# Optimization experiments

Measured on AMD Instinct MI355X. Metric: run time of the kernel, lower is better.

## Reference

```python
import jax, jax.numpy as jnp
import numpy as np

B, S, D, H = 2, 2048, 1024, 16
DK = D // H


def setup_inputs() -> dict:
    key = jax.random.key(0)
    ks = jax.random.split(key, 9)
    def xavier(k, shape):
        fan_in, fan_out = shape[1], shape[0]
        lim = jnp.sqrt(6.0 / (fan_in + fan_out))
        return jax.random.uniform(k, shape, jnp.float32, -lim, lim)
    x = jax.random.normal(ks[0], (B, S, D), jnp.float32)
    mask = jnp.ones((B, 1, S), jnp.int32)
    Wq = xavier(ks[1], (D, D)); bq = jnp.zeros((D,), jnp.float32)
    Wk = xavier(ks[2], (D, D)); bk = jnp.zeros((D,), jnp.float32)
    Wv = xavier(ks[3], (D, D)); bv = jnp.zeros((D,), jnp.float32)
    Wo = xavier(ks[4], (D, D)); bo = jnp.zeros((D,), jnp.float32)
    return {"x": x, "mask": mask, "Wq": Wq, "bq": bq, "Wk": Wk, "bk": bk,
            "Wv": Wv, "bv": bv, "Wo": Wo, "bo": bo}


def reference(x, mask, Wq, bq, Wk, bk, Wv, bv, Wo, bo):
    # Linear layers use torch convention y = x @ W.T + b
    q = (x @ Wq.T + bq).reshape(B, S, H, DK).transpose(0, 2, 1, 3)  # [B,H,S,DK]
    k = (x @ Wk.T + bk).reshape(B, S, H, DK).transpose(0, 2, 1, 3)
    v = (x @ Wv.T + bv).reshape(B, S, H, DK).transpose(0, 2, 1, 3)
    scores = jnp.einsum('bhqd,bhkd->bhqk', q, k) / jnp.sqrt(jnp.float32(DK))
    m = mask[:, None, :, :]  # unsqueeze(1): broadcast over heads -> [B,1,1,S]
    scores = jnp.where(m == 0, jnp.float32(-1e9), scores)
    p = jax.nn.softmax(scores, axis=-1)  # dropout p=0.0 -> identity
    ctx = jnp.einsum('bhqk,bhkd->bhqd', p, v)
    ctx = ctx.transpose(0, 2, 1, 3).reshape(B, S, D)
    return ctx @ Wo.T + bo
```

## Files before the change

### kernel.cpp

```cpp
#include <hip/hip_runtime.h>
#include <hip/hip_bf16.h>
#include <math.h>

#define Bn 2
#define Sn 2048
#define Dn 1024
#define Hn 16
#define DKn 64
#define BHS (Bn * Hn * Sn)

using fragb  = __attribute__((ext_vector_type(8))) short;
using frag16 = __attribute__((ext_vector_type(8))) _Float16;
using f4     = __attribute__((ext_vector_type(4))) float;

__device__ __forceinline__ short f2bf(float f) {
    union { float f; unsigned u; } v; v.f = f;
    unsigned r = v.u + 0x7FFF + ((v.u >> 16) & 1);
    return (short)(r >> 16);
}
__device__ __forceinline__ unsigned short f2h(float f) {
    _Float16 h = (_Float16)f;
    unsigned short s; __builtin_memcpy(&s, &h, 2); return s;
}

#define GLOAD(gptr, lptr)                                                     \
    __builtin_amdgcn_global_load_lds(                                         \
        (const __attribute__((address_space(1))) unsigned int*)(const void*)(gptr), \
        (__attribute__((address_space(3))) unsigned int*)(void*)(lptr), 16, 0, 0)

#define NX (Bn * Sn * Dn)
#define NW (Dn * Dn)
#define NF4 ((NX + 4 * NW) / 4)

__global__ __launch_bounds__(256) void prep(
    const float* __restrict__ x,  const float* __restrict__ Wq,
    const float* __restrict__ Wk, const float* __restrict__ Wv,
    const float* __restrict__ Wo, const int* __restrict__ mask,
    short* __restrict__ xh,
    short* __restrict__ Wqh, short* __restrict__ Wkh,
    short* __restrict__ Wvh, short* __restrict__ Woh,
    short* __restrict__ mfb)
{
    int i = blockIdx.x * 256 + threadIdx.x;
    if (i < NF4) {
        int e = i << 2;
        const float* src; short* dst; int j;
        if (e < NX)               { src = x;  dst = xh;  j = e; }
        else if (e < NX + NW)     { src = Wq; dst = Wqh; j = e - NX; }
        else if (e < NX + 2 * NW) { src = Wk; dst = Wkh; j = e - NX - NW; }
        else if (e < NX + 3 * NW) { src = Wv; dst = Wvh; j = e - NX - 2 * NW; }
        else                      { src = Wo; dst = Woh; j = e - NX - 3 * NW; }
        float4 v = *(const float4*)(src + j);
        ushort4 o;
        o.x = f2h(v.x); o.y = f2h(v.y); o.z = f2h(v.z); o.w = f2h(v.w);
        *(ushort4*)(dst + j) = o;
    } else {
        int j = (i - NF4) << 2;
        if (j < Bn * Sn) {
            int4 m = *(const int4*)(mask + j);
            ushort4 o;
            o.x = m.x ? 0x3F80 : 0; o.y = m.y ? 0x3F80 : 0;
            o.z = m.z ? 0x3F80 : 0; o.w = m.w ? 0x3F80 : 0;
            *(ushort4*)(mfb + j) = o;
        }
    }
}

__global__ __launch_bounds__(256) void gemm_qkv(
    const short* __restrict__ A,
    const short* __restrict__ W0, const float* __restrict__ b0,
    const short* __restrict__ W1, const float* __restrict__ b1,
    const short* __restrict__ W2, const float* __restrict__ b2,
    const int* __restrict__ mask,
    short* __restrict__ Qb, short* __restrict__ Kb, short* __restrict__ Vtb)
{
    __shared__ __align__(16) short As[128 * 32];
    __shared__ __align__(16) short Bs[128 * 32];

    const int tid  = threadIdx.x;
    const int wave = tid >> 6;
    const int lane = tid & 63;
    const int quad = lane >> 4;
    const int l16  = lane & 15;
    const int wm   = wave >> 1;
    const int wn   = wave & 1;

    const int m0   = blockIdx.y * 128;
    const int n0   = blockIdx.x * 128;
    const int widx = n0 >> 10;
    const int nl0  = n0 & 1023;

    const short* Wp   = widx == 0 ? W0 : (widx == 1 ? W1 : W2);
    const float* bias = widx == 0 ? b0 : (widx == 1 ? b1 : b2);

    f4 acc[4][4];
    #pragma unroll
    for (int i = 0; i < 4; i++)
        #pragma unroll
        for (int j = 0; j < 4; j++) {
            acc[i][j][0] = 0.f; acc[i][j][1] = 0.f;
            acc[i][j][2] = 0.f; acc[i][j][3] = 0.f;
        }

    const int K = Dn;
    const int r0  = tid >> 2,         kc0 = (tid & 3) * 8;
    const int r1  = (tid + 256) >> 2;
    const short* Ar0 = A  + (size_t)(m0 + r0) * K + kc0;
    const short* Ar1 = A  + (size_t)(m0 + r1) * K + kc0;
    const short* Br0 = Wp + (size_t)(nl0 + r0) * K + kc0;
    const short* Br1 = Wp + (size_t)(nl0 + r1) * K + kc0;

    for (int k0 = 0; k0 < K; k0 += 32) {
        __syncthreads();
        GLOAD(Ar0 + k0, &As[(wave * 64) * 8]);
        GLOAD(Ar1 + k0, &As[(256 + wave * 64) * 8]);
        GLOAD(Br0 + k0, &Bs[(wave * 64) * 8]);
        GLOAD(Br1 + k0, &Bs[(256 + wave * 64) * 8]);
        __syncthreads();

        frag16 a[4], b[4];
        #pragma unroll
        for (int mi = 0; mi < 4; mi++)
            a[mi] = *(const frag16*)&As[(wm * 64 + mi * 16 + l16) * 32 + quad * 8];
        #pragma unroll
        for (int ni = 0; ni < 4; ni++)
            b[ni] = *(const frag16*)&Bs[(wn * 64 + ni * 16 + l16) * 32 + quad * 8];
        #pragma unroll
        for (int mi = 0; mi < 4; mi++)
            #pragma unroll
            for (int ni = 0; ni < 4; ni++)
                acc[mi][ni] = __builtin_amdgcn_mfma_f32_16x16x32_f16(
                    a[mi], b[ni], acc[mi][ni], 0, 0, 0);
    }

    const float QSCALE = 0.125f * 1.44269504088896340736f;

    #pragma unroll
    for (int mi = 0; mi < 4; mi++) {
        #pragma unroll
        for (int ni = 0; ni < 4; ni++) {
            int nl = nl0 + wn * 64 + ni * 16 + l16;
            float bv = bias[nl];
            #pragma unroll
            for (int r = 0; r < 4; r++) {
                int m = m0 + wm * 64 + mi * 16 + quad * 4 + r;
                float v = acc[mi][ni][r] + bv;
                int b  = m >> 11, s = m & (Sn - 1);
                int h  = nl >> 6, dk = nl & 63;
                if (widx == 0)
                    Qb[((size_t)(b * Hn + h) * Sn + s) * DKn + dk] = f2bf(v * QSCALE);
                else if (widx == 1)
                    Kb[((size_t)(b * Hn + h) * Sn + s) * DKn + dk] = f2bf(v);
                else {
                    float mv = (float)mask[b * Sn + s];
                    Vtb[((size_t)(b * Hn + h) * DKn + dk) * Sn + s] = f2bf(v * mv);
                }
            }
        }
    }
}

__global__ __launch_bounds__(256) void gemm_out(
    const short* __restrict__ A, const short* __restrict__ Wp,
    const float* __restrict__ bias, float* __restrict__ outf)
{
    __shared__ __align__(16) short As[64 * 32];
    __shared__ __align__(16) short Bs[128 * 32];

    const int tid  = threadIdx.x;
    const int wave = tid >> 6;
    const int lane = tid & 63;
    const int quad = lane >> 4;
    const int l16  = lane & 15;
    const int wm   = wave >> 1;
    const int wn   = wave & 1;

    const int m0 = blockIdx.y * 64;
    const int n0 = blockIdx.x * 128;

    f4 acc[2][4];
    #pragma unroll
    for (int i = 0; i < 2; i++)
        #pragma unroll
        for (int j = 0; j < 4; j++) {
            acc[i][j][0] = 0.f; acc[i][j][1] = 0.f;
            acc[i][j][2] = 0.f; acc[i][j][3] = 0.f;
        }

    const int K = Dn;
    const int r0  = tid >> 2,         kc0 = (tid & 3) * 8;
    const int r1  = (tid + 256) >> 2;
    const short* Ar0 = A  + (size_t)(m0 + r0) * K + kc0;
    const short* Br0 = Wp + (size_t)(n0 + r0) * K + kc0;
    const short* Br1 = Wp + (size_t)(n0 + r1) * K + kc0;

    for (int k0 = 0; k0 < K; k0 += 32) {
        __syncthreads();
        GLOAD(Ar0 + k0, &As[(wave * 64) * 8]);
        GLOAD(Br0 + k0, &Bs[(wave * 64) * 8]);
        GLOAD(Br1 + k0, &Bs[(256 + wave * 64) * 8]);
        __syncthreads();

        frag16 a[2], b[4];
        #pragma unroll
        for (int mi = 0; mi < 2; mi++)
            a[mi] = *(const frag16*)&As[(wm * 32 + mi * 16 + l16) * 32 + quad * 8];
        #pragma unroll
        for (int ni = 0; ni < 4; ni++)
            b[ni] = *(const frag16*)&Bs[(wn * 64 + ni * 16 + l16) * 32 + quad * 8];
        #pragma unroll
        for (int mi = 0; mi < 2; mi++)
            #pragma unroll
            for (int ni = 0; ni < 4; ni++)
                acc[mi][ni] = __builtin_amdgcn_mfma_f32_16x16x32_f16(
                    a[mi], b[ni], acc[mi][ni], 0, 0, 0);
    }

    #pragma unroll
    for (int mi = 0; mi < 2; mi++) {
        #pragma unroll
        for (int ni = 0; ni < 4; ni++) {
            int nl = n0 + wn * 64 + ni * 16 + l16;
            float bv = bias[nl];
            #pragma unroll
            for (int r = 0; r < 4; r++) {
                int m = m0 + wm * 32 + mi * 16 + quad * 4 + r;
                outf[(size_t)m * Dn + nl] = acc[mi][ni][r] + bv;
            }
        }
    }
}

#define LP  72

__global__ __launch_bounds__(256) void attn_mfma(
    const short* __restrict__ Qb, const short* __restrict__ Kb,
    const short* __restrict__ Vtb, const short* __restrict__ mfb,
    float* __restrict__ ctxp0, float* __restrict__ ctxp1,
    float* __restrict__ lp)
{
    __shared__ __align__(16) short Ks[64 * 64];
    __shared__ __align__(16) short Vs[64 * 64];
    __shared__ short Ps[4][32 * LP];
    __shared__ __align__(16) short mfs[64];

    const int tid  = threadIdx.x;
    const int wave = tid >> 6;
    const int lane = tid & 63;
    const int quad = lane >> 4;
    const int l16  = lane & 15;

    const int split = blockIdx.x & 1;
    const int rest  = blockIdx.x >> 1;
    const int qt  = rest & 15;
    const int bhh = rest >> 4;
    const int b   = bhh >> 4;
    const int h   = bhh & 15;

    fragb qf[2][2];
    #pragma unroll
    for (int w = 0; w < 2; w++) {
        int qrow = qt * 128 + wave * 32 + w * 16 + l16;
        const short* qptr = Qb + ((size_t)bhh * Sn + qrow) * DKn + quad * 8;
        qf[w][0] = *(const fragb*)(qptr);
        qf[w][1] = *(const fragb*)(qptr + 32);
    }

    f4 ctx[2][4];
    #pragma unroll
    for (int w = 0; w < 2; w++)
        #pragma unroll
        for (int dt = 0; dt < 4; dt++) {
            ctx[w][dt][0] = 0.f; ctx[w][dt][1] = 0.f;
            ctx[w][dt][2] = 0.f; ctx[w][dt][3] = 0.f;
        }
    f4 lacc[2];
    lacc[0][0] = 0.f; lacc[0][1] = 0.f; lacc[0][2] = 0.f; lacc[0][3] = 0.f;
    lacc[1] = lacc[0];

    const int lr = lane >> 3;
    const int sc = ((lane & 7) ^ lr) * 8;
    const short* Kg = Kb  + (size_t)bhh * Sn * DKn;
    const short* Vg = Vtb + (size_t)bhh * DKn * Sn;
    const short* mg = mfb + (size_t)b * Sn;

    const short* Ksrc = Kg + (size_t)(wave * 16 + lr) * DKn + sc;
    const short* Vsrc = Vg + (size_t)(wave * 16 + lr) * Sn + sc;

    const int c0 = ((quad ^ (l16 & 7)) * 8);

    const int kt0 = split * 16;
    for (int kt = kt0; kt < kt0 + 16; kt++) {
        __syncthreads();
        GLOAD(Ksrc + (size_t)kt * 4096,             &Ks[(wave * 16) * 64]);
        GLOAD(Ksrc + (size_t)kt * 4096 + 8 * DKn,   &Ks[(wave * 16 + 8) * 64]);
        GLOAD(Vsrc + (size_t)kt * 64,               &Vs[(wave * 16) * 64]);
        GLOAD(Vsrc + (size_t)kt * 64 + 8 * Sn,      &Vs[(wave * 16 + 8) * 64]);
        if (tid < 8)
            *(uint4*)&mfs[tid * 8] = *(const uint4*)(mg + kt * 64 + tid * 8);
        __syncthreads();

        #pragma unroll
        for (int t = 0; t < 4; t++) {
            fragb k0 = *(const fragb*)&Ks[(t * 16 + l16) * 64 + c0];
            fragb k1 = *(const fragb*)&Ks[(t * 16 + l16) * 64 + (c0 ^ 32)];
            #pragma unroll
            for (int w = 0; w < 2; w++) {
                f4 a; a[0] = 0.f; a[1] = 0.f; a[2] = 0.f; a[3] = 0.f;
                a = __builtin_amdgcn_mfma_f32_16x16x32_bf16(k0, qf[w][0], a, 0, 0, 0);
                a = __builtin_amdgcn_mfma_f32_16x16x32_bf16(k1, qf[w][1], a, 0, 0, 0);
                unsigned u0 = __float_as_uint(__builtin_amdgcn_exp2f(a[0]));
                unsigned u1 = __float_as_uint(__builtin_amdgcn_exp2f(a[1]));
                unsigned u2 = __float_as_uint(__builtin_amdgcn_exp2f(a[2]));
                unsigned u3 = __float_as_uint(__builtin_amdgcn_exp2f(a[3]));
                uint2 pw;
                pw.x = __builtin_amdgcn_perm(u1, u0, 0x07060302u);
                pw.y = __builtin_amdgcn_perm(u3, u2, 0x07060302u);
                *(uint2*)&Ps[wave][(w * 16 + l16) * LP + 16 * t + quad * 4] = pw;
            }
        }

        fragb p[2][2];
        #pragma unroll
        for (int w = 0; w < 2; w++) {
            p[w][0] = *(const fragb*)&Ps[wave][(w * 16 + l16) * LP + quad * 8];
            p[w][1] = *(const fragb*)&Ps[wave][(w * 16 + l16) * LP + quad * 8 + 32];
        }
        fragb m0 = *(const fragb*)&mfs[quad * 8];
        fragb m1 = *(const fragb*)&mfs[quad * 8 + 32];
        #pragma unroll
        for (int w = 0; w < 2; w++) {
            lacc[w] = __builtin_amdgcn_mfma_f32_16x16x32_bf16(p[w][0], m0, lacc[w], 0, 0, 0);
            lacc[w] = __builtin_amdgcn_mfma_f32_16x16x32_bf16(p[w][1], m1, lacc[w], 0, 0, 0);
        }
        #pragma unroll
        for (int dt = 0; dt < 4; dt++) {
            fragb v0 = *(const fragb*)&Vs[(dt * 16 + l16) * 64 + c0];
            fragb v1 = *(const fragb*)&Vs[(dt * 16 + l16) * 64 + (c0 ^ 32)];
            #pragma unroll
            for (int w = 0; w < 2; w++) {
                ctx[w][dt] = __builtin_amdgcn_mfma_f32_16x16x32_bf16(p[w][0], v0, ctx[w][dt], 0, 0, 0);
                ctx[w][dt] = __builtin_amdgcn_mfma_f32_16x16x32_bf16(p[w][1], v1, ctx[w][dt], 0, 0, 0);
            }
        }
    }

    float* cp  = split ? ctxp1 : ctxp0;
    float* lpp = lp + (size_t)split * BHS;
    #pragma unroll
    for (int w = 0; w < 2; w++)
        #pragma unroll
        for (int r = 0; r < 4; r++) {
            int row = qt * 128 + wave * 32 + w * 16 + quad * 4 + r;
            if (l16 == 0) lpp[(size_t)bhh * Sn + row] = lacc[w][r];
            #pragma unroll
            for (int dt = 0; dt < 4; dt++)
                cp[((size_t)(b * Sn + row)) * Dn + h * DKn + dt * 16 + l16] =
                    ctx[w][dt][r];
        }
}

__global__ __launch_bounds__(256) void reduce_ctx(
    const float* __restrict__ c0, const float* __restrict__ c1,
    const float* __restrict__ lp, short* __restrict__ Ch)
{
    int i4 = blockIdx.x * 256 + threadIdx.x;
    int e    = i4 << 2;
    int brow = e >> 10;
    int d    = e & 1023;
    int b    = brow >> 11;
    int row  = brow & (Sn - 1);
    int h    = d >> 6;
    size_t li = (size_t)(b * Hn + h) * Sn + row;
    float l = lp[li] + lp[BHS + li];
    float inv = 1.f / l;
    float4 v0 = ((const float4*)c0)[i4];
    float4 v1 = ((const float4*)c1)[i4];
    ushort4 o;
    o.x = f2h((v0.x + v1.x) * inv);
    o.y = f2h((v0.y + v1.y) * inv);
    o.z = f2h((v0.z + v1.z) * inv);
    o.w = f2h((v0.w + v1.w) * inv);
    ((ushort4*)Ch)[i4] = o;
}

extern "C" void kernel_launch(void* const* d_in, const int* in_sizes, int n_in,
                              void* d_out, int out_size, void* d_ws, size_t ws_size,
                              hipStream_t stream) {
    const float* x    = (const float*)d_in[0];
    const int*   mask = (const int*)d_in[1];
    const float* Wq   = (const float*)d_in[2];
    const float* bq   = (const float*)d_in[3];
    const float* Wk   = (const float*)d_in[4];
    const float* bk   = (const float*)d_in[5];
    const float* Wv   = (const float*)d_in[6];
    const float* bv   = (const float*)d_in[7];
    const float* Wo   = (const float*)d_in[8];
    const float* bo   = (const float*)d_in[9];
    float* out = (float*)d_out;

    char* ws = (char*)d_ws;
    const size_t MB = 1024u * 1024u;
    short* xh    = (short*)(ws + 0 * MB);
    short* Wqh   = (short*)(ws + 8 * MB);
    short* Wkh   = (short*)(ws + 10 * MB);
    short* Wvh   = (short*)(ws + 12 * MB);
    short* Qb    = (short*)(ws + 16 * MB);
    short* Kb    = (short*)(ws + 24 * MB);
    short* Vtb   = (short*)(ws + 32 * MB);
    float* ctxp0 = (float*)(ws + 0 * MB);
    float* ctxp1 = (float*)(ws + 40 * MB);
    short* Woh   = (short*)(ws + 56 * MB);
    float* lp    = (float*)(ws + 58 * MB);
    short* mfb   = (short*)(ws + 59 * MB);
    short* Ch    = (short*)(ws + 60 * MB);

    const int PRE = NF4 + (Bn * Sn) / 4;
    prep<<<(PRE + 255) / 256, 256, 0, stream>>>(
        x, Wq, Wk, Wv, Wo, mask, xh, Wqh, Wkh, Wvh, Woh, mfb);

    gemm_qkv<<<dim3(24, 32), 256, 0, stream>>>(
        xh, Wqh, bq, Wkh, bk, Wvh, bv, mask, Qb, Kb, Vtb);

    attn_mfma<<<dim3(Bn * Hn * (Sn / 128) * 2), 256, 0, stream>>>(
        Qb, Kb, Vtb, mfb, ctxp0, ctxp1, lp);

    reduce_ctx<<<dim3(NX / 4 / 256), 256, 0, stream>>>(ctxp0, ctxp1, lp, Ch);

    gemm_out<<<dim3(8, 64), 256, 0, stream>>>(Ch, Woh, bo, out);
}
```

Baseline: 213.0 us.

## Double-buffer GEMM LDS tiles with K=64 stages and XOR swizzle

Both projection GEMMs now prefetch the next 64-wide K slice into a second LDS buffer while computing on the current one. A single barrier per iteration replaces the previous pair, and an XOR swizzle on LDS columns reduces bank conflicts. The output GEMM tile grows to 128x128 with a halved grid. LDS usage rises to 64KB per block, which may reduce occupancy, and the larger out-GEMM tile gives fewer blocks (256) to spread across CUs.

```diff
diff --git a/kernel.cpp b/kernel.cpp
--- a/kernel.cpp
+++ b/kernel.cpp
@@ -66,6 +66,45 @@
     }
 }
 
+
+#define STAGE(buf, kk0) do {                                                  \
+    const short* _as = Asrc + (kk0);                                          \
+    const short* _bs = Bsrc + (kk0);                                          \
+    GLOAD(_as,            &As[buf][wave * 512]);                              \
+    GLOAD(_as + 32 * Dn,  &As[buf][2048 + wave * 512]);                       \
+    GLOAD(_as + 64 * Dn,  &As[buf][4096 + wave * 512]);                       \
+    GLOAD(_as + 96 * Dn,  &As[buf][6144 + wave * 512]);                       \
+    GLOAD(_bs,            &Bs[buf][wave * 512]);                              \
+    GLOAD(_bs + 32 * Dn,  &Bs[buf][2048 + wave * 512]);                       \
+    GLOAD(_bs + 64 * Dn,  &Bs[buf][4096 + wave * 512]);                       \
+    GLOAD(_bs + 96 * Dn,  &Bs[buf][6144 + wave * 512]);                       \
+} while (0)
+
+#define COMPUTE(buf) do {                                                     \
+    frag16 _a[2][4], _b[2][4];                                                \
+    _Pragma("unroll")                                                         \
+    for (int kk = 0; kk < 2; kk++) {                                          \
+        _Pragma("unroll")                                                     \
+        for (int mi = 0; mi < 4; mi++)                                        \
+            _a[kk][mi] = *(const frag16*)&As[buf][                            \
+                (wm * 64 + mi * 16 + l16) * 64 +                              \
+                (((kk << 2) | quad) ^ (l16 & 7)) * 8];                        \
+        _Pragma("unroll")                                                     \
+        for (int ni = 0; ni < 4; ni++)                                        \
+            _b[kk][ni] = *(const frag16*)&Bs[buf][                            \
+                (wn * 64 + ni * 16 + l16) * 64 +                              \
+                (((kk << 2) | quad) ^ (l16 & 7)) * 8];                        \
+    }                                                                         \
+    _Pragma("unroll")                                                         \
+    for (int kk = 0; kk < 2; kk++)                                            \
+        _Pragma("unroll")                                                     \
+        for (int mi = 0; mi < 4; mi++)                                        \
+            _Pragma("unroll")                                                 \
+            for (int ni = 0; ni < 4; ni++)                                    \
+                acc[mi][ni] = __builtin_amdgcn_mfma_f32_16x16x32_f16(         \
+                    _a[kk][mi], _b[kk][ni], acc[mi][ni], 0, 0, 0);            \
+} while (0)
+
 __global__ __launch_bounds__(256) void gemm_qkv(
     const short* __restrict__ A,
     const short* __restrict__ W0, const float* __restrict__ b0,
@@ -74,8 +113,8 @@
     const int* __restrict__ mask,
     short* __restrict__ Qb, short* __restrict__ Kb, short* __restrict__ Vtb)
 {
-    __shared__ __align__(16) short As[128 * 32];
-    __shared__ __align__(16) short Bs[128 * 32];
+    __shared__ __align__(16) short As[2][128 * 64];
+    __shared__ __align__(16) short Bs[2][128 * 64];
 
     const int tid  = threadIdx.x;
     const int wave = tid >> 6;
@@ -102,36 +141,21 @@
             acc[i][j][2] = 0.f; acc[i][j][3] = 0.f;
         }
 
-    const int K = Dn;
-    const int r0  = tid >> 2,         kc0 = (tid & 3) * 8;
-    const int r1  = (tid + 256) >> 2;
-    const short* Ar0 = A  + (size_t)(m0 + r0) * K + kc0;
-    const short* Ar1 = A  + (size_t)(m0 + r1) * K + kc0;
-    const short* Br0 = Wp + (size_t)(nl0 + r0) * K + kc0;
-    const short* Br1 = Wp + (size_t)(nl0 + r1) * K + kc0;
-
-    for (int k0 = 0; k0 < K; k0 += 32) {
+    const int sr = tid >> 3;
+    const int sc = ((tid & 7) ^ (sr & 7)) * 8;
+    const short* Asrc = A  + (size_t)(m0  + sr) * Dn + sc;
+    const short* Bsrc = Wp + (size_t)(nl0 + sr) * Dn + sc;
+
+    STAGE(0, 0);
+    __syncthreads();
+    int cur = 0;
+    for (int it = 0; it < 15; ++it) {
+        STAGE(cur ^ 1, (it + 1) << 6);
+        COMPUTE(cur);
         __syncthreads();
-        GLOAD(Ar0 + k0, &As[(wave * 64) * 8]);
-        GLOAD(Ar1 + k0, &As[(256 + wave * 64) * 8]);
-        GLOAD(Br0 + k0, &Bs[(wave * 64) * 8]);
-        GLOAD(Br1 + k0, &Bs[(256 + wave * 64) * 8]);
-        __syncthreads();
-
-        frag16 a[4], b[4];
-        #pragma unroll
-        for (int mi = 0; mi < 4; mi++)
-            a[mi] = *(const frag16*)&As[(wm * 64 + mi * 16 + l16) * 32 + quad * 8];
-        #pragma unroll
-        for (int ni = 0; ni < 4; ni++)
-            b[ni] = *(const frag16*)&Bs[(wn * 64 + ni * 16 + l16) * 32 + quad * 8];
-        #pragma unroll
-        for (int mi = 0; mi < 4; mi++)
-            #pragma unroll
-            for (int ni = 0; ni < 4; ni++)
-                acc[mi][ni] = __builtin_amdgcn_mfma_f32_16x16x32_f16(
-                    a[mi], b[ni], acc[mi][ni], 0, 0, 0);
-    }
+        cur ^= 1;
+    }
+    COMPUTE(cur);
 
     const float QSCALE = 0.125f * 1.44269504088896340736f;
 
@@ -164,8 +188,8 @@
     const short* __restrict__ A, const short* __restrict__ Wp,
     const float* __restrict__ bias, float* __restrict__ outf)
 {
-    __shared__ __align__(16) short As[64 * 32];
-    __shared__ __align__(16) short Bs[128 * 32];
+    __shared__ __align__(16) short As[2][128 * 64];
+    __shared__ __align__(16) short Bs[2][128 * 64];
 
     const int tid  = threadIdx.x;
     const int wave = tid >> 6;
@@ -175,56 +199,43 @@
     const int wm   = wave >> 1;
     const int wn   = wave & 1;
 
-    const int m0 = blockIdx.y * 64;
+    const int m0 = blockIdx.y * 128;
     const int n0 = blockIdx.x * 128;
 
-    f4 acc[2][4];
-    #pragma unroll
-    for (int i = 0; i < 2; i++)
+    f4 acc[4][4];
+    #pragma unroll
+    for (int i = 0; i < 4; i++)
         #pragma unroll
         for (int j = 0; j < 4; j++) {
             acc[i][j][0] = 0.f; acc[i][j][1] = 0.f;
             acc[i][j][2] = 0.f; acc[i][j][3] = 0.f;
         }
 
-    const int K = Dn;
-    const int r0  = tid >> 2,         kc0 = (tid & 3) * 8;
-    const int r1  = (tid + 256) >> 2;
-    const short* Ar0 = A  + (size_t)(m0 + r0) * K + kc0;
-    const short* Br0 = Wp + (size_t)(n0 + r0) * K + kc0;
-    const short* Br1 = Wp + (size_t)(n0 + r1) * K + kc0;
-
-    for (int k0 = 0; k0 < K; k0 += 32) {
+    const int sr = tid >> 3;
+    const int sc = ((tid & 7) ^ (sr & 7)) * 8;
+    const short* Asrc = A  + (size_t)(m0 + sr) * Dn + sc;
+    const short* Bsrc = Wp + (size_t)(n0 + sr) * Dn + sc;
+
+    STAGE(0, 0);
+    __syncthreads();
+    int cur = 0;
+    for (int it = 0; it < 15; ++it) {
+        STAGE(cur ^ 1, (it + 1) << 6);
+        COMPUTE(cur);
         __syncthreads();
-        GLOAD(Ar0 + k0, &As[(wave * 64) * 8]);
-        GLOAD(Br0 + k0, &Bs[(wave * 64) * 8]);
-        GLOAD(Br1 + k0, &Bs[(256 + wave * 64) * 8]);
-        __syncthreads();
-
-        frag16 a[2], b[4];
-        #pragma unroll
-        for (int mi = 0; mi < 2; mi++)
-            a[mi] = *(const frag16*)&As[(wm * 32 + mi * 16 + l16) * 32 + quad * 8];
-        #pragma unroll
-        for (int ni = 0; ni < 4; ni++)
-            b[ni] = *(const frag16*)&Bs[(wn * 64 + ni * 16 + l16) * 32 + quad * 8];
-        #pragma unroll
-        for (int mi = 0; mi < 2; mi++)
-            #pragma unroll
-            for (int ni = 0; ni < 4; ni++)
-                acc[mi][ni] = __builtin_amdgcn_mfma_f32_16x16x32_f16(
-                    a[mi], b[ni], acc[mi][ni], 0, 0, 0);
-    }
-
-    #pragma unroll
-    for (int mi = 0; mi < 2; mi++) {
+        cur ^= 1;
+    }
+    COMPUTE(cur);
+
+    #pragma unroll
+    for (int mi = 0; mi < 4; mi++) {
         #pragma unroll
         for (int ni = 0; ni < 4; ni++) {
             int nl = n0 + wn * 64 + ni * 16 + l16;
             float bv = bias[nl];
             #pragma unroll
             for (int r = 0; r < 4; r++) {
-                int m = m0 + wm * 32 + mi * 16 + quad * 4 + r;
+                int m = m0 + wm * 64 + mi * 16 + quad * 4 + r;
                 outf[(size_t)m * Dn + nl] = acc[mi][ni][r] + bv;
             }
         }
@@ -427,5 +438,5 @@
 
     reduce_ctx<<<dim3(NX / 4 / 256), 256, 0, stream>>>(ctxp0, ctxp1, lp, Ch);
 
-    gemm_out<<<dim3(8, 64), 256, 0, stream>>>(Ch, Woh, bo, out);
-}
+    gemm_out<<<dim3(8, 32), 256, 0, stream>>>(Ch, Woh, bo, out);
+}
```

Measured after the change: 235.5 us. 1.11x slower.

## Shrink GEMM tiles and XOR-swizzle LDS layout to avoid bank conflicts

Applied to the files above, without the earlier changes.

The QKV projection GEMM tile drops from 128x128 to 64x128 and the output GEMM tile from 64x128 to 64x64, doubling the grid sizes to 1536 and 1024 blocks. This gives more blocks for the 256 compute units and uses fewer accumulator registers. The LDS fill and fragment reads now XOR-swizzle the 8-element column chunk by row bits, to reduce LDS bank conflicts on the 16-byte fragment loads. The cost is lower data reuse per block, so more global and L2 traffic for the same GEMM.

```diff
diff --git a/kernel.cpp b/kernel.cpp
--- a/kernel.cpp
+++ b/kernel.cpp
@@ -66,6 +66,7 @@
     }
 }
 
+
 __global__ __launch_bounds__(256) void gemm_qkv(
     const short* __restrict__ A,
     const short* __restrict__ W0, const float* __restrict__ b0,
@@ -74,7 +75,7 @@
     const int* __restrict__ mask,
     short* __restrict__ Qb, short* __restrict__ Kb, short* __restrict__ Vtb)
 {
-    __shared__ __align__(16) short As[128 * 32];
+    __shared__ __align__(16) short As[64 * 32];
     __shared__ __align__(16) short Bs[128 * 32];
 
     const int tid  = threadIdx.x;
@@ -85,7 +86,7 @@
     const int wm   = wave >> 1;
     const int wn   = wave & 1;
 
-    const int m0   = blockIdx.y * 128;
+    const int m0   = blockIdx.y * 64;
     const int n0   = blockIdx.x * 128;
     const int widx = n0 >> 10;
     const int nl0  = n0 & 1023;
@@ -93,40 +94,40 @@
     const short* Wp   = widx == 0 ? W0 : (widx == 1 ? W1 : W2);
     const float* bias = widx == 0 ? b0 : (widx == 1 ? b1 : b2);
 
-    f4 acc[4][4];
-    #pragma unroll
-    for (int i = 0; i < 4; i++)
+    f4 acc[2][4];
+    #pragma unroll
+    for (int i = 0; i < 2; i++)
         #pragma unroll
         for (int j = 0; j < 4; j++) {
             acc[i][j][0] = 0.f; acc[i][j][1] = 0.f;
             acc[i][j][2] = 0.f; acc[i][j][3] = 0.f;
         }
 
-    const int K = Dn;
-    const int r0  = tid >> 2,         kc0 = (tid & 3) * 8;
-    const int r1  = (tid + 256) >> 2;
-    const short* Ar0 = A  + (size_t)(m0 + r0) * K + kc0;
-    const short* Ar1 = A  + (size_t)(m0 + r1) * K + kc0;
-    const short* Br0 = Wp + (size_t)(nl0 + r0) * K + kc0;
-    const short* Br1 = Wp + (size_t)(nl0 + r1) * K + kc0;
+    const int K  = Dn;
+    const int r0 = tid >> 2;
+    const int sc = ((tid & 3) ^ ((tid >> 3) & 3)) * 8;
+    const short* Ar0 = A  + (size_t)(m0  + r0)      * K + sc;
+    const short* Br0 = Wp + (size_t)(nl0 + r0)      * K + sc;
+    const short* Br1 = Wp + (size_t)(nl0 + r0 + 64) * K + sc;
+
+    const int cA = (quad ^ ((l16 >> 1) & 3)) * 8;
 
     for (int k0 = 0; k0 < K; k0 += 32) {
         __syncthreads();
-        GLOAD(Ar0 + k0, &As[(wave * 64) * 8]);
-        GLOAD(Ar1 + k0, &As[(256 + wave * 64) * 8]);
-        GLOAD(Br0 + k0, &Bs[(wave * 64) * 8]);
-        GLOAD(Br1 + k0, &Bs[(256 + wave * 64) * 8]);
-        __syncthreads();
-
-        frag16 a[4], b[4];
-        #pragma unroll
-        for (int mi = 0; mi < 4; mi++)
-            a[mi] = *(const frag16*)&As[(wm * 64 + mi * 16 + l16) * 32 + quad * 8];
+        GLOAD(Ar0 + k0, &As[wave * 512]);
+        GLOAD(Br0 + k0, &Bs[wave * 512]);
+        GLOAD(Br1 + k0, &Bs[2048 + wave * 512]);
+        __syncthreads();
+
+        frag16 a[2], b[4];
+        #pragma unroll
+        for (int mi = 0; mi < 2; mi++)
+            a[mi] = *(const frag16*)&As[(wm * 32 + mi * 16 + l16) * 32 + cA];
         #pragma unroll
         for (int ni = 0; ni < 4; ni++)
-            b[ni] = *(const frag16*)&Bs[(wn * 64 + ni * 16 + l16) * 32 + quad * 8];
-        #pragma unroll
-        for (int mi = 0; mi < 4; mi++)
+            b[ni] = *(const frag16*)&Bs[(wn * 64 + ni * 16 + l16) * 32 + cA];
+        #pragma unroll
+        for (int mi = 0; mi < 2; mi++)
             #pragma unroll
             for (int ni = 0; ni < 4; ni++)
                 acc[mi][ni] = __builtin_amdgcn_mfma_f32_16x16x32_f16(
@@ -136,14 +137,14 @@
     const float QSCALE = 0.125f * 1.44269504088896340736f;
 
     #pragma unroll
-    for (int mi = 0; mi < 4; mi++) {
+    for (int mi = 0; mi < 2; mi++) {
         #pragma unroll
         for (int ni = 0; ni < 4; ni++) {
             int nl = nl0 + wn * 64 + ni * 16 + l16;
             float bv = bias[nl];
             #pragma unroll
             for (int r = 0; r < 4; r++) {
-                int m = m0 + wm * 64 + mi * 16 + quad * 4 + r;
+                int m = m0 + wm * 32 + mi * 16 + quad * 4 + r;
                 float v = acc[mi][ni][r] + bv;
                 int b  = m >> 11, s = m & (Sn - 1);
                 int h  = nl >> 6, dk = nl & 63;
@@ -165,7 +166,7 @@
     const float* __restrict__ bias, float* __restrict__ outf)
 {
     __shared__ __align__(16) short As[64 * 32];
-    __shared__ __align__(16) short Bs[128 * 32];
+    __shared__ __align__(16) short Bs[64 * 32];
 
     const int tid  = threadIdx.x;
     const int wave = tid >> 6;
@@ -176,42 +177,42 @@
     const int wn   = wave & 1;
 
     const int m0 = blockIdx.y * 64;
-    const int n0 = blockIdx.x * 128;
-
-    f4 acc[2][4];
+    const int n0 = blockIdx.x * 64;
+
+    f4 acc[2][2];
     #pragma unroll
     for (int i = 0; i < 2; i++)
         #pragma unroll
-        for (int j = 0; j < 4; j++) {
+        for (int j = 0; j < 2; j++) {
             acc[i][j][0] = 0.f; acc[i][j][1] = 0.f;
             acc[i][j][2] = 0.f; acc[i][j][3] = 0.f;
         }
 
-    const int K = Dn;
-    const int r0  = tid >> 2,         kc0 = (tid & 3) * 8;
-    const int r1  = (tid + 256) >> 2;
-    const short* Ar0 = A  + (size_t)(m0 + r0) * K + kc0;
-    const short* Br0 = Wp + (size_t)(n0 + r0) * K + kc0;
-    const short* Br1 = Wp + (size_t)(n0 + r1) * K + kc0;
+    const int K  = Dn;
+    const int r0 = tid >> 2;
+    const int sc = ((tid & 3) ^ ((tid >> 3) & 3)) * 8;
+    const short* Ao0 = A  + (size_t)(m0 + r0) * K + sc;
+    const short* Bo0 = Wp + (size_t)(n0 + r0) * K + sc;
+
+    const int cA = (quad ^ ((l16 >> 1) & 3)) * 8;
 
     for (int k0 = 0; k0 < K; k0 += 32) {
         __syncthreads();
-        GLOAD(Ar0 + k0, &As[(wave * 64) * 8]);
-        GLOAD(Br0 + k0, &Bs[(wave * 64) * 8]);
-        GLOAD(Br1 + k0, &Bs[(256 + wave * 64) * 8]);
-        __syncthreads();
-
-        frag16 a[2], b[4];
+        GLOAD(Ao0 + k0, &As[wave * 512]);
+        GLOAD(Bo0 + k0, &Bs[wave * 512]);
+        __syncthreads();
+
+        frag16 a[2], b[2];
         #pragma unroll
         for (int mi = 0; mi < 2; mi++)
-            a[mi] = *(const frag16*)&As[(wm * 32 + mi * 16 + l16) * 32 + quad * 8];
-        #pragma unroll
-        for (int ni = 0; ni < 4; ni++)
-            b[ni] = *(const frag16*)&Bs[(wn * 64 + ni * 16 + l16) * 32 + quad * 8];
+            a[mi] = *(const frag16*)&As[(wm * 32 + mi * 16 + l16) * 32 + cA];
+        #pragma unroll
+        for (int ni = 0; ni < 2; ni++)
+            b[ni] = *(const frag16*)&Bs[(wn * 32 + ni * 16 + l16) * 32 + cA];
         #pragma unroll
         for (int mi = 0; mi < 2; mi++)
             #pragma unroll
-            for (int ni = 0; ni < 4; ni++)
+            for (int ni = 0; ni < 2; ni++)
                 acc[mi][ni] = __builtin_amdgcn_mfma_f32_16x16x32_f16(
                     a[mi], b[ni], acc[mi][ni], 0, 0, 0);
     }
@@ -219,8 +220,8 @@
     #pragma unroll
     for (int mi = 0; mi < 2; mi++) {
         #pragma unroll
-        for (int ni = 0; ni < 4; ni++) {
-            int nl = n0 + wn * 64 + ni * 16 + l16;
+        for (int ni = 0; ni < 2; ni++) {
+            int nl = n0 + wn * 32 + ni * 16 + l16;
             float bv = bias[nl];
             #pragma unroll
             for (int r = 0; r < 4; r++) {
@@ -419,7 +420,7 @@
     prep<<<(PRE + 255) / 256, 256, 0, stream>>>(
         x, Wq, Wk, Wv, Wo, mask, xh, Wqh, Wkh, Wvh, Woh, mfb);
 
-    gemm_qkv<<<dim3(24, 32), 256, 0, stream>>>(
+    gemm_qkv<<<dim3(24, 64), 256, 0, stream>>>(
         xh, Wqh, bq, Wkh, bk, Wvh, bv, mask, Qb, Kb, Vtb);
 
     attn_mfma<<<dim3(Bn * Hn * (Sn / 128) * 2), 256, 0, stream>>>(
@@ -427,5 +428,5 @@
 
     reduce_ctx<<<dim3(NX / 4 / 256), 256, 0, stream>>>(ctxp0, ctxp1, lp, Ch);
 
-    gemm_out<<<dim3(8, 64), 256, 0, stream>>>(Ch, Woh, bo, out);
-}
+    gemm_out<<<dim3(16, 64), 256, 0, stream>>>(Ch, Woh, bo, out);
+}
```

Measured after the change: 223.7 us. 5.0% more time.

## Triple-buffer QKV GEMM shared-memory tiles with XOR-swizzled LDS layout

Applied to the files above, without the earlier changes.

Replaces the single-buffered K loop of the QKV projection GEMM with a three-stage pipeline. Global-to-LDS loads run two tiles ahead, and partial vmcnt waits plus barriers let loads overlap the MFMA work. It also XOR-swizzles the column chunk in both the load and the fragment read to cut LDS bank conflicts. This triples LDS use per block, which may lower occupancy.

```diff
diff --git a/kernel.cpp b/kernel.cpp
--- a/kernel.cpp
+++ b/kernel.cpp
@@ -74,8 +74,12 @@
     const int* __restrict__ mask,
     short* __restrict__ Qb, short* __restrict__ Kb, short* __restrict__ Vtb)
 {
-    __shared__ __align__(16) short As[128 * 32];
-    __shared__ __align__(16) short Bs[128 * 32];
+    __shared__ __align__(16) short As0[128 * 32];
+    __shared__ __align__(16) short Bs0[128 * 32];
+    __shared__ __align__(16) short As1[128 * 32];
+    __shared__ __align__(16) short Bs1[128 * 32];
+    __shared__ __align__(16) short As2[128 * 32];
+    __shared__ __align__(16) short Bs2[128 * 32];
 
     const int tid  = threadIdx.x;
     const int wave = tid >> 6;
@@ -102,36 +106,67 @@
             acc[i][j][2] = 0.f; acc[i][j][3] = 0.f;
         }
 
-    const int K = Dn;
-    const int r0  = tid >> 2,         kc0 = (tid & 3) * 8;
-    const int r1  = (tid + 256) >> 2;
-    const short* Ar0 = A  + (size_t)(m0 + r0) * K + kc0;
-    const short* Ar1 = A  + (size_t)(m0 + r1) * K + kc0;
-    const short* Br0 = Wp + (size_t)(nl0 + r0) * K + kc0;
-    const short* Br1 = Wp + (size_t)(nl0 + r1) * K + kc0;
-
-    for (int k0 = 0; k0 < K; k0 += 32) {
-        __syncthreads();
-        GLOAD(Ar0 + k0, &As[(wave * 64) * 8]);
-        GLOAD(Ar1 + k0, &As[(256 + wave * 64) * 8]);
-        GLOAD(Br0 + k0, &Bs[(wave * 64) * 8]);
-        GLOAD(Br1 + k0, &Bs[(256 + wave * 64) * 8]);
-        __syncthreads();
-
-        frag16 a[4], b[4];
-        #pragma unroll
-        for (int mi = 0; mi < 4; mi++)
-            a[mi] = *(const frag16*)&As[(wm * 64 + mi * 16 + l16) * 32 + quad * 8];
-        #pragma unroll
-        for (int ni = 0; ni < 4; ni++)
-            b[ni] = *(const frag16*)&Bs[(wn * 64 + ni * 16 + l16) * 32 + quad * 8];
-        #pragma unroll
-        for (int mi = 0; mi < 4; mi++)
-            #pragma unroll
-            for (int ni = 0; ni < 4; ni++)
-                acc[mi][ni] = __builtin_amdgcn_mfma_f32_16x16x32_f16(
-                    a[mi], b[ni], acc[mi][ni], 0, 0, 0);
-    }
+    const int K  = Dn;
+    const int r0 = tid >> 2;
+    const int sc = ((tid & 3) ^ ((tid >> 3) & 3)) * 8;
+    const short* Ar0 = A  + (size_t)(m0  + r0)      * K + sc;
+    const short* Ar1 = A  + (size_t)(m0  + r0 + 64) * K + sc;
+    const short* Br0 = Wp + (size_t)(nl0 + r0)      * K + sc;
+    const short* Br1 = Wp + (size_t)(nl0 + r0 + 64) * K + sc;
+
+    const int cA = (quad ^ ((l16 >> 1) & 3)) * 8;
+
+#define STAGEQ(AS, BS, kk) do {                                               \
+    GLOAD(Ar0 + (kk), &AS[wave * 512]);                                       \
+    GLOAD(Ar1 + (kk), &AS[2048 + wave * 512]);                                \
+    GLOAD(Br0 + (kk), &BS[wave * 512]);                                       \
+    GLOAD(Br1 + (kk), &BS[2048 + wave * 512]);                                \
+} while (0)
+
+#define COMPUTEQ(AS, BS) do {                                                 \
+    frag16 a_[4], b_[4];                                                      \
+    _Pragma("unroll")                                                         \
+    for (int mi = 0; mi < 4; mi++)                                            \
+        a_[mi] = *(const frag16*)&AS[(wm * 64 + mi * 16 + l16) * 32 + cA];    \
+    _Pragma("unroll")                                                         \
+    for (int ni = 0; ni < 4; ni++)                                            \
+        b_[ni] = *(const frag16*)&BS[(wn * 64 + ni * 16 + l16) * 32 + cA];    \
+    _Pragma("unroll")                                                         \
+    for (int mi = 0; mi < 4; mi++)                                            \
+        _Pragma("unroll")                                                     \
+        for (int ni = 0; ni < 4; ni++)                                        \
+            acc[mi][ni] = __builtin_amdgcn_mfma_f32_16x16x32_f16(             \
+                a_[mi], b_[ni], acc[mi][ni], 0, 0, 0);                        \
+} while (0)
+
+#define KSTEP(CA, CB, SA, SB, kk, VN) do {                                    \
+    STAGEQ(SA, SB, kk);                                                       \
+    asm volatile("s_waitcnt vmcnt(" #VN ")" ::: "memory");                    \
+    __builtin_amdgcn_sched_barrier(0);                                        \
+    __builtin_amdgcn_s_barrier();                                             \
+    COMPUTEQ(CA, CB);                                                         \
+    __builtin_amdgcn_sched_barrier(0);                                        \
+    __builtin_amdgcn_s_barrier();                                             \
+} while (0)
+
+#define KSTEP_LAST(CA, CB, VN) do {                                           \
+    asm volatile("s_waitcnt vmcnt(" #VN ")" ::: "memory");                    \
+    __builtin_amdgcn_sched_barrier(0);                                        \
+    __builtin_amdgcn_s_barrier();                                             \
+    COMPUTEQ(CA, CB);                                                         \
+    __builtin_amdgcn_sched_barrier(0);                                        \
+    __builtin_amdgcn_s_barrier();                                             \
+} while (0)
+
+    STAGEQ(As0, Bs0, 0);
+    STAGEQ(As1, Bs1, 32);
+    for (int k0 = 0; k0 < 960; k0 += 96) {
+        KSTEP(As0, Bs0, As2, Bs2, k0 + 64, 8);
+        KSTEP(As1, Bs1, As0, Bs0, k0 + 96, 8);
+        KSTEP(As2, Bs2, As1, Bs1, k0 + 128, 8);
+    }
+    KSTEP_LAST(As0, Bs0, 4);
+    KSTEP_LAST(As1, Bs1, 0);
 
     const float QSCALE = 0.125f * 1.44269504088896340736f;
 
```

Result: slower. 229.0 us (+7.5%).
